# Kernel tuning notes

Hardware: AMD Instinct MI355X
Metric: run time of the kernel (lower is better)

Reference implementation:

```python
import jax, jax.numpy as jnp
import numpy as np

B, C, H, W = 32, 512, 32, 32
CI = C // 2  # inter_channels
EPS = 1e-5


def setup_inputs() -> dict:
    key = jax.random.key(0)
    ks = jax.random.split(key, 12)
    s = 0.02
    return {
        "x": jax.random.normal(ks[0], (B, C, H, W), jnp.float32),
        "w_g": jax.random.normal(ks[1], (CI, C), jnp.float32) * s,
        "b_g": jax.random.normal(ks[2], (CI,), jnp.float32) * s,
        "w_theta": jax.random.normal(ks[3], (CI, C), jnp.float32) * s,
        "b_theta": jax.random.normal(ks[4], (CI,), jnp.float32) * s,
        "w_phi": jax.random.normal(ks[5], (CI, C), jnp.float32) * s,
        "b_phi": jax.random.normal(ks[6], (CI,), jnp.float32) * s,
        "w_W": jax.random.normal(ks[7], (C, CI), jnp.float32) * s,
        "b_W": jax.random.normal(ks[8], (C,), jnp.float32) * s,
        "bn_gamma": jax.random.normal(ks[9], (C,), jnp.float32) * 0.1 + 1.0,
        "bn_beta": jax.random.normal(ks[10], (C,), jnp.float32) * 0.1,
        "bn_mean": jax.random.normal(ks[11], (C,), jnp.float32) * 0.1,
        "bn_var": jnp.abs(jax.random.normal(jax.random.fold_in(key, 99), (C,), jnp.float32)) * 0.5 + 0.5,
    }


def reference(x, w_g, b_g, w_theta, b_theta, w_phi, b_phi, w_W, b_W,
              bn_gamma, bn_beta, bn_mean, bn_var):
    b, c, h, w = x.shape
    n = h * w
    xf = x.reshape(b, c, n)  # [B, C, N]
    # 1x1 convs == per-pixel channel matmuls
    g = jnp.einsum('oc,bcn->bon', w_g, xf) + b_g[:, None]          # [B, Ci, N]
    theta = jnp.einsum('oc,bcn->bon', w_theta, xf) + b_theta[:, None]
    phi = jnp.einsum('oc,bcn->bon', w_phi, xf) + b_phi[:, None]
    # f[b, i, j] = theta_i . phi_j ; scaled by 1/N (softmax-free attention)
    f_div_C = jnp.einsum('bcn,bcm->bnm', theta, phi) / n           # [B, N, N]
    # y[b, c, n] = sum_m f[b, n, m] * g[b, c, m]
    y = jnp.einsum('bnm,bcm->bcn', f_div_C, g)                     # [B, Ci, N]
    # W: 1x1 conv back to C channels + BatchNorm (inference form)
    Wy = jnp.einsum('oi,bin->bon', w_W, y) + b_W[:, None]          # [B, C, N]
    inv_std = jax.lax.rsqrt(bn_var + EPS)
    bn = (Wy - bn_mean[:, None]) * (inv_std * bn_gamma)[:, None] + bn_beta[:, None]
    z = bn.reshape(b, c, h, w) + x
    return z
```

## Files before the change

kernel.cpp:

```cpp
#include <hip/hip_runtime.h>
#include <hip/hip_bf16.h>
#include <cstdint>
#include <cstddef>

using bf16 = __hip_bfloat16;
typedef __attribute__((ext_vector_type(8))) short short8v;
typedef __attribute__((ext_vector_type(4))) float f32x4;

static constexpr int BATCH = 32;
static constexpr int CH    = 512;
static constexpr int CIc   = 256;
static constexpr int NSP   = 1024;
#define EPSV 1e-5f

__device__ __forceinline__ bf16 f2bf(float f) { return __float2bfloat16(f); }

__device__ __forceinline__ void gload_lds16(const bf16* g, bf16* l) {
  __builtin_amdgcn_global_load_lds(
      (const __attribute__((address_space(1))) void*)g,
      (__attribute__((address_space(3))) void*)l, 16, 0, 0);
}

__global__ __launch_bounds__(256) void convert_weights(
    const float* __restrict__ wg, const float* __restrict__ wph, const float* __restrict__ wth,
    const float* __restrict__ bg, const float* __restrict__ bph, const float* __restrict__ bth,
    const float* __restrict__ wW,
    bf16* __restrict__ wcat, bf16* __restrict__ wWb, float* __restrict__ biascat)
{
  int i = blockIdx.x * 256 + threadIdx.x;
  const int WSZ = CIc * CH;
  if (i < WSZ) {
    wcat[i]         = f2bf(wg[i]);
    wcat[WSZ + i]   = f2bf(wph[i]);
    wcat[2*WSZ + i] = f2bf(wth[i]);
    wWb[i]          = f2bf(wW[i]);
  }
  if (i < CIc) {
    biascat[i]        = bg[i];
    biascat[CIc + i]  = bph[i];
    biascat[2*CIc + i]= bth[i];
  }
}

__global__ __launch_bounds__(256) void transpose_x_kernel(
    const float* __restrict__ x, bf16* __restrict__ xt)
{
  __shared__ bf16 t[32][34];
  int n0 = blockIdx.x * 32, c0 = blockIdx.y * 32, b = blockIdx.z;
  const float* s = x + (size_t)b * CH * NSP;
  bf16* d = xt + (size_t)b * NSP * CH;
  int tx = threadIdx.x & 31, ty = threadIdx.x >> 5;
  #pragma unroll
  for (int i = 0; i < 32; i += 8)
    t[ty + i][tx] = f2bf(s[(size_t)(c0 + ty + i) * NSP + n0 + tx]);
  __syncthreads();
  #pragma unroll
  for (int i = 0; i < 32; i += 8)
    d[(size_t)(n0 + ty + i) * CH + c0 + tx] = t[tx][ty + i];
}

template<int EPI>
__global__ __launch_bounds__(256) void gemm_nt(
    const bf16* __restrict__ A, size_t sA,
    const bf16* __restrict__ Bm, size_t sB,
    void* __restrict__ Cm, size_t sC,
    int M, int N, int K,
    const float* __restrict__ bias,
    bf16* __restrict__ Tt, size_t sT,
    const float* __restrict__ bW, const float* __restrict__ gma,
    const float* __restrict__ bta, const float* __restrict__ mu,
    const float* __restrict__ var,
    const float* __restrict__ xres, size_t sX)
{
  __shared__ bf16 As[2][128 * 64];
  __shared__ bf16 Bs[2][128 * 64];
  const int b  = blockIdx.z;
  const int m0 = blockIdx.y * 128;
  const int n0 = blockIdx.x * 128;
  const bf16* Ab = A  + (size_t)b * sA;
  const bf16* Bb = Bm + (size_t)b * sB;
  const int tid  = threadIdx.x;
  const int wv   = tid >> 6, lane = tid & 63;
  const int l16  = lane & 15, g4 = lane >> 4;
  const int wr   = wv >> 1,  wc = wv & 1;

  f32x4 acc[4][4];
  #pragma unroll
  for (int i = 0; i < 4; ++i)
    #pragma unroll
    for (int j = 0; j < 4; ++j)
      acc[i][j] = (f32x4){0.f, 0.f, 0.f, 0.f};

  auto stage = [&](int ks, int p) {
    #pragma unroll
    for (int i = 0; i < 4; ++i) {
      int s = i * 256 + tid;
      int row = s >> 3, ch8 = (s & 7) << 3;
      gload_lds16(Ab + (size_t)(m0 + row) * K + ks + ch8, &As[p][(i * 256 + wv * 64) * 8]);
      gload_lds16(Bb + (size_t)(n0 + row) * K + ks + ch8, &Bs[p][(i * 256 + wv * 64) * 8]);
    }
  };

  const int nt = K >> 6;
  stage(0, 0);
  __syncthreads();
  for (int t = 0; t < nt; ++t) {
    const int cur = t & 1;
    if (t + 1 < nt) stage((t + 1) << 6, cur ^ 1);
    #pragma unroll
    for (int kk = 0; kk < 2; ++kk) {
      short8v af[4], bfv[4];
      #pragma unroll
      for (int mf = 0; mf < 4; ++mf)
        af[mf] = *(const short8v*)&As[cur][(wr * 64 + mf * 16 + l16) * 64 + kk * 32 + g4 * 8];
      #pragma unroll
      for (int nf = 0; nf < 4; ++nf)
        bfv[nf] = *(const short8v*)&Bs[cur][(wc * 64 + nf * 16 + l16) * 64 + kk * 32 + g4 * 8];
      #pragma unroll
      for (int mf = 0; mf < 4; ++mf)
        #pragma unroll
        for (int nf = 0; nf < 4; ++nf)
          acc[mf][nf] = __builtin_amdgcn_mfma_f32_16x16x32_bf16(af[mf], bfv[nf], acc[mf][nf], 0, 0, 0);
    }
    __syncthreads();
  }

  const int colbase = n0 + wc * 64 + l16;
  const int rowbase = m0 + wr * 64 + g4 * 4;

  if constexpr (EPI == 2) {
    #pragma unroll
    for (int mf = 0; mf < 4; ++mf) {
      #pragma unroll
      for (int j = 0; j < 4; ++j) {
        int row = rowbase + mf * 16 + j;
        float a  = gma[row] * rsqrtf(var[row] + EPSV);
        float bb = (bW[row] - mu[row]) * a + bta[row];
        float sc = a * (1.f / (float)NSP);
        #pragma unroll
        for (int nf = 0; nf < 4; ++nf) {
          int col = colbase + nf * 16;
          ((float*)Cm)[(size_t)b * sC + (size_t)row * N + col] =
              acc[mf][nf][j] * sc + bb + xres[(size_t)b * sX + (size_t)row * N + col];
        }
      }
    }
  } else if constexpr (EPI == 1) {
    if (m0 >= 512) {
      #pragma unroll
      for (int mf = 0; mf < 4; ++mf) {
        int rowt0 = (m0 - 512) + wr * 64 + mf * 16 + g4 * 4;
        #pragma unroll
        for (int nf = 0; nf < 4; ++nf) {
          int col = colbase + nf * 16;
          uint64_t pk = 0;
          #pragma unroll
          for (int j = 0; j < 4; ++j) {
            bf16 bv = f2bf(acc[mf][nf][j] + bias[512 + rowt0 + j]);
            pk |= (uint64_t)(*(unsigned short*)&bv) << (16 * j);
          }
          *(uint64_t*)(Tt + (size_t)b * sT + (size_t)col * CIc + rowt0) = pk;
        }
      }
    } else {
      #pragma unroll
      for (int mf = 0; mf < 4; ++mf)
        #pragma unroll
        for (int j = 0; j < 4; ++j) {
          int row = rowbase + mf * 16 + j;
          float badd = bias[row];
          #pragma unroll
          for (int nf = 0; nf < 4; ++nf) {
            int col = colbase + nf * 16;
            ((bf16*)Cm)[(size_t)b * sC + (size_t)row * N + col] = f2bf(acc[mf][nf][j] + badd);
          }
        }
    }
  } else {
    #pragma unroll
    for (int mf = 0; mf < 4; ++mf)
      #pragma unroll
      for (int j = 0; j < 4; ++j) {
        int row = rowbase + mf * 16 + j;
        #pragma unroll
        for (int nf = 0; nf < 4; ++nf) {
          int col = colbase + nf * 16;
          ((bf16*)Cm)[(size_t)b * sC + (size_t)row * N + col] = f2bf(acc[mf][nf][j]);
        }
      }
  }
}

extern "C" void kernel_launch(void* const* d_in, const int* in_sizes, int n_in,
                              void* d_out, int out_size, void* d_ws, size_t ws_size,
                              hipStream_t stream)
{
  const float* x    = (const float*)d_in[0];
  const float* w_g  = (const float*)d_in[1];
  const float* b_g  = (const float*)d_in[2];
  const float* w_th = (const float*)d_in[3];
  const float* b_th = (const float*)d_in[4];
  const float* w_ph = (const float*)d_in[5];
  const float* b_ph = (const float*)d_in[6];
  const float* w_W  = (const float*)d_in[7];
  const float* b_W  = (const float*)d_in[8];
  const float* gma  = (const float*)d_in[9];
  const float* bta  = (const float*)d_in[10];
  const float* mu   = (const float*)d_in[11];
  const float* var  = (const float*)d_in[12];
  float* out = (float*)d_out;

  char* ws = (char*)d_ws;
  bf16* proj = (bf16*)(ws + 0);
  bf16* xt   = (bf16*)(ws + 33554432);
  bf16* thT  = (bf16*)(ws + 67108864);
  bf16* S    = (bf16*)(ws + 83886080);
  bf16* T    = (bf16*)(ws + 88080384);
  bf16* wcat = (bf16*)(ws + 96468992);
  bf16* wWb  = (bf16*)(ws + 97255424);
  float* bcat= (float*)(ws + 97517568);

  convert_weights<<<512, 256, 0, stream>>>(w_g, w_ph, w_th, b_g, b_ph, b_th, w_W, wcat, wWb, bcat);
  transpose_x_kernel<<<dim3(32, 16, 32), 256, 0, stream>>>(x, xt);

  gemm_nt<1><<<dim3(8, 6, 32), 256, 0, stream>>>(
      wcat, 0, xt, (size_t)NSP * CH, proj, (size_t)CH * NSP,
      768, NSP, CH, bcat, thT, (size_t)NSP * CIc,
      nullptr, nullptr, nullptr, nullptr, nullptr, nullptr, 0);

  gemm_nt<0><<<dim3(2, 2, 32), 256, 0, stream>>>(
      proj + 256 * 1024, (size_t)CH * NSP, proj, (size_t)CH * NSP, S, (size_t)CIc * CIc,
      CIc, CIc, NSP, nullptr, nullptr, 0,
      nullptr, nullptr, nullptr, nullptr, nullptr, nullptr, 0);

  gemm_nt<0><<<dim3(2, 4, 32), 256, 0, stream>>>(
      wWb, 0, S, (size_t)CIc * CIc, T, (size_t)CH * CIc,
      CH, CIc, CIc, nullptr, nullptr, 0,
      nullptr, nullptr, nullptr, nullptr, nullptr, nullptr, 0);

  gemm_nt<2><<<dim3(8, 4, 32), 256, 0, stream>>>(
      T, (size_t)CH * CIc, thT, (size_t)NSP * CIc, out, (size_t)CH * NSP,
      CH, NSP, CIc, nullptr, nullptr, 0,
      b_W, gma, bta, mu, var, x, (size_t)CH * NSP);
}
```

Measured before the change: 138.6 us.

## Use 256x256 tiled 8-wave GEMM with swizzled LDS and split-K-half pipelining

Adds a new 512-thread GEMM kernel with 256x256 output tiles, XOR-swizzled LDS layout, half-tile staged prefetch with explicit vmcnt waits, and MFMA priority hints. It is used for the projection GEMM and the final output GEMM. The projection GEMM now treats batch as part of the N dimension, giving one 128x3 grid over the whole batch. The goal is more data reuse per block and less LDS bank conflict, at the cost of one block per CU and fewer total blocks in the final GEMM (256).

Measured after the change: 135.4 us. -2.3%, faster.

```diff
diff --git a/kernel.cpp b/kernel.cpp
--- a/kernel.cpp
+++ b/kernel.cpp
@@ -60,17 +60,164 @@
 }
 
 template<int EPI>
-__global__ __launch_bounds__(256) void gemm_nt(
+__global__ __launch_bounds__(512, 1) void gemm_nt_256(
     const bf16* __restrict__ A, size_t sA,
     const bf16* __restrict__ Bm, size_t sB,
-    void* __restrict__ Cm, size_t sC,
-    int M, int N, int K,
+    void* __restrict__ Cm,
+    int K,
     const float* __restrict__ bias,
-    bf16* __restrict__ Tt, size_t sT,
+    bf16* __restrict__ Tt,
     const float* __restrict__ bW, const float* __restrict__ gma,
     const float* __restrict__ bta, const float* __restrict__ mu,
     const float* __restrict__ var,
-    const float* __restrict__ xres, size_t sX)
+    const float* __restrict__ xres)
+{
+  __shared__ bf16 As[2][2][256][32];
+  __shared__ bf16 Bs[2][2][256][32];
+  const int zb = blockIdx.z;
+  const int m0 = blockIdx.y * 256;
+  const int n0 = blockIdx.x * 256;
+  const bf16* Ab = A  + (size_t)zb * sA;
+  const bf16* Bb = Bm + (size_t)zb * sB;
+  const int tid  = threadIdx.x;
+  const int wv   = tid >> 6, lane = tid & 63;
+  const int l16  = lane & 15, g4 = lane >> 4;
+  const int wr   = wv >> 2,  wc = wv & 3;
+
+  f32x4 acc[8][4];
+  #pragma unroll
+  for (int i = 0; i < 8; ++i)
+    #pragma unroll
+    for (int j = 0; j < 4; ++j)
+      acc[i][j] = (f32x4){0.f, 0.f, 0.f, 0.f};
+
+  const int swz = ((lane & 3) ^ ((lane >> 3) & 3)) << 3;
+  const int rl  = lane >> 2;
+  auto SH = [&](int tt, int h, int p) {
+    int kbase = tt * 64 + h * 32 + swz;
+    #pragma unroll
+    for (int q = 0; q < 2; ++q) {
+      int r = wv * 32 + q * 16;
+      gload_lds16(Ab + (size_t)(m0 + r + rl) * K + kbase, &As[p][h][r][0]);
+      gload_lds16(Bb + (size_t)(n0 + r + rl) * K + kbase, &Bs[p][h][r][0]);
+    }
+  };
+
+  short8v af[8], bfr[4];
+  const int rslot = (g4 ^ ((l16 >> 1) & 3)) * 8;
+  auto LOADFRAGS = [&](int d, int h) {
+    #pragma unroll
+    for (int mf = 0; mf < 8; ++mf)
+      af[mf] = *(const short8v*)&As[d][h][wr * 128 + mf * 16 + l16][rslot];
+    #pragma unroll
+    for (int nf = 0; nf < 4; ++nf)
+      bfr[nf] = *(const short8v*)&Bs[d][h][wc * 64 + nf * 16 + l16][rslot];
+  };
+  auto MFMAS = [&]() {
+    __builtin_amdgcn_s_setprio(1);
+    #pragma unroll
+    for (int mf = 0; mf < 8; ++mf)
+      #pragma unroll
+      for (int nf = 0; nf < 4; ++nf)
+        acc[mf][nf] = __builtin_amdgcn_mfma_f32_16x16x32_bf16(af[mf], bfr[nf], acc[mf][nf], 0, 0, 0);
+    __builtin_amdgcn_s_setprio(0);
+  };
+
+  const int nt = K >> 6;
+  SH(0, 0, 0); SH(0, 1, 0); SH(1, 0, 1);
+  for (int t = 0; t < nt - 1; ++t) {
+    const int d = t & 1;
+    __builtin_amdgcn_sched_barrier(0);
+    asm volatile("s_waitcnt vmcnt(8)" ::: "memory");
+    __builtin_amdgcn_s_barrier();
+    __builtin_amdgcn_sched_barrier(0);
+    LOADFRAGS(d, 0);
+    SH(t + 1, 1, d ^ 1);
+    MFMAS();
+    __builtin_amdgcn_sched_barrier(0);
+    asm volatile("s_waitcnt vmcnt(8)" ::: "memory");
+    __builtin_amdgcn_s_barrier();
+    __builtin_amdgcn_sched_barrier(0);
+    LOADFRAGS(d, 1);
+    if (t + 2 < nt) SH(t + 2, 0, d);
+    MFMAS();
+    __builtin_amdgcn_sched_barrier(0);
+  }
+  {
+    const int d = (nt - 1) & 1;
+    asm volatile("s_waitcnt vmcnt(4)" ::: "memory");
+    __builtin_amdgcn_s_barrier();
+    __builtin_amdgcn_sched_barrier(0);
+    LOADFRAGS(d, 0);
+    MFMAS();
+    asm volatile("s_waitcnt vmcnt(0)" ::: "memory");
+    __builtin_amdgcn_s_barrier();
+    __builtin_amdgcn_sched_barrier(0);
+    LOADFRAGS(d, 1);
+    MFMAS();
+  }
+
+  const int colbase = n0 + wc * 64 + l16;
+  const int rowb    = wr * 128 + g4 * 4;
+
+  if constexpr (EPI == 2) {
+    #pragma unroll
+    for (int mf = 0; mf < 8; ++mf) {
+      #pragma unroll
+      for (int j = 0; j < 4; ++j) {
+        int row = m0 + rowb + mf * 16 + j;
+        float a  = gma[row] * rsqrtf(var[row] + EPSV);
+        float bb = (bW[row] - mu[row]) * a + bta[row];
+        float sc = a * (1.f / (float)NSP);
+        #pragma unroll
+        for (int nf = 0; nf < 4; ++nf) {
+          int col = colbase + nf * 16;
+          size_t idx = (size_t)zb * (CH * NSP) + (size_t)row * NSP + col;
+          ((float*)Cm)[idx] = acc[mf][nf][j] * sc + bb + ((const float*)xres)[idx];
+        }
+      }
+    }
+  } else {
+    if (m0 < 512) {
+      #pragma unroll
+      for (int mf = 0; mf < 8; ++mf)
+        #pragma unroll
+        for (int j = 0; j < 4; ++j) {
+          int row = m0 + rowb + mf * 16 + j;
+          float badd = bias[row];
+          #pragma unroll
+          for (int nf = 0; nf < 4; ++nf) {
+            int col = colbase + nf * 16;
+            int b = col >> 10, n = col & 1023;
+            ((bf16*)Cm)[(size_t)b * (CH * NSP) + (size_t)row * NSP + n] = f2bf(acc[mf][nf][j] + badd);
+          }
+        }
+    } else {
+      #pragma unroll
+      for (int mf = 0; mf < 8; ++mf) {
+        int ci0 = rowb + mf * 16;
+        #pragma unroll
+        for (int nf = 0; nf < 4; ++nf) {
+          int col = colbase + nf * 16;
+          int b = col >> 10, n = col & 1023;
+          uint64_t pk = 0;
+          #pragma unroll
+          for (int j = 0; j < 4; ++j) {
+            bf16 bv = f2bf(acc[mf][nf][j] + bias[512 + ci0 + j]);
+            pk |= (uint64_t)(*(unsigned short*)&bv) << (16 * j);
+          }
+          *(uint64_t*)(Tt + (size_t)b * (NSP * CIc) + (size_t)n * CIc + ci0) = pk;
+        }
+      }
+    }
+  }
+}
+
+__global__ __launch_bounds__(256) void gemm_nt_small(
+    const bf16* __restrict__ A, size_t sA,
+    const bf16* __restrict__ Bm, size_t sB,
+    bf16* __restrict__ Cm, size_t sC,
+    int N, int K)
 {
   __shared__ bf16 As[2][128 * 64];
   __shared__ bf16 Bs[2][128 * 64];
@@ -127,68 +274,17 @@
 
   const int colbase = n0 + wc * 64 + l16;
   const int rowbase = m0 + wr * 64 + g4 * 4;
-
-  if constexpr (EPI == 2) {
-    #pragma unroll
-    for (int mf = 0; mf < 4; ++mf) {
-      #pragma unroll
-      for (int j = 0; j < 4; ++j) {
-        int row = rowbase + mf * 16 + j;
-        float a  = gma[row] * rsqrtf(var[row] + EPSV);
-        float bb = (bW[row] - mu[row]) * a + bta[row];
-        float sc = a * (1.f / (float)NSP);
-        #pragma unroll
-        for (int nf = 0; nf < 4; ++nf) {
-          int col = colbase + nf * 16;
-          ((float*)Cm)[(size_t)b * sC + (size_t)row * N + col] =
-              acc[mf][nf][j] * sc + bb + xres[(size_t)b * sX + (size_t)row * N + col];
-        }
+  #pragma unroll
+  for (int mf = 0; mf < 4; ++mf)
+    #pragma unroll
+    for (int j = 0; j < 4; ++j) {
+      int row = rowbase + mf * 16 + j;
+      #pragma unroll
+      for (int nf = 0; nf < 4; ++nf) {
+        int col = colbase + nf * 16;
+        Cm[(size_t)b * sC + (size_t)row * N + col] = f2bf(acc[mf][nf][j]);
       }
     }
-  } else if constexpr (EPI == 1) {
-    if (m0 >= 512) {
-      #pragma unroll
-      for (int mf = 0; mf < 4; ++mf) {
-        int rowt0 = (m0 - 512) + wr * 64 + mf * 16 + g4 * 4;
-        #pragma unroll
-        for (int nf = 0; nf < 4; ++nf) {
-          int col = colbase + nf * 16;
-          uint64_t pk = 0;
-          #pragma unroll
-          for (int j = 0; j < 4; ++j) {
-            bf16 bv = f2bf(acc[mf][nf][j] + bias[512 + rowt0 + j]);
-            pk |= (uint64_t)(*(unsigned short*)&bv) << (16 * j);
-          }
-          *(uint64_t*)(Tt + (size_t)b * sT + (size_t)col * CIc + rowt0) = pk;
-        }
-      }
-    } else {
-      #pragma unroll
-      for (int mf = 0; mf < 4; ++mf)
-        #pragma unroll
-        for (int j = 0; j < 4; ++j) {
-          int row = rowbase + mf * 16 + j;
-          float badd = bias[row];
-          #pragma unroll
-          for (int nf = 0; nf < 4; ++nf) {
-            int col = colbase + nf * 16;
-            ((bf16*)Cm)[(size_t)b * sC + (size_t)row * N + col] = f2bf(acc[mf][nf][j] + badd);
-          }
-        }
-    }
-  } else {
-    #pragma unroll
-    for (int mf = 0; mf < 4; ++mf)
-      #pragma unroll
-      for (int j = 0; j < 4; ++j) {
-        int row = rowbase + mf * 16 + j;
-        #pragma unroll
-        for (int nf = 0; nf < 4; ++nf) {
-          int col = colbase + nf * 16;
-          ((bf16*)Cm)[(size_t)b * sC + (size_t)row * N + col] = f2bf(acc[mf][nf][j]);
-        }
-      }
-  }
 }
 
 extern "C" void kernel_launch(void* const* d_in, const int* in_sizes, int n_in,
@@ -223,23 +319,19 @@
   convert_weights<<<512, 256, 0, stream>>>(w_g, w_ph, w_th, b_g, b_ph, b_th, w_W, wcat, wWb, bcat);
   transpose_x_kernel<<<dim3(32, 16, 32), 256, 0, stream>>>(x, xt);
 
-  gemm_nt<1><<<dim3(8, 6, 32), 256, 0, stream>>>(
-      wcat, 0, xt, (size_t)NSP * CH, proj, (size_t)CH * NSP,
-      768, NSP, CH, bcat, thT, (size_t)NSP * CIc,
-      nullptr, nullptr, nullptr, nullptr, nullptr, nullptr, 0);
-
-  gemm_nt<0><<<dim3(2, 2, 32), 256, 0, stream>>>(
+  gemm_nt_256<1><<<dim3(128, 3, 1), 512, 0, stream>>>(
+      wcat, 0, xt, 0, proj, CH, bcat, thT,
+      nullptr, nullptr, nullptr, nullptr, nullptr, nullptr);
+
+  gemm_nt_small<<<dim3(2, 2, 32), 256, 0, stream>>>(
       proj + 256 * 1024, (size_t)CH * NSP, proj, (size_t)CH * NSP, S, (size_t)CIc * CIc,
-      CIc, CIc, NSP, nullptr, nullptr, 0,
-      nullptr, nullptr, nullptr, nullptr, nullptr, nullptr, 0);
-
-  gemm_nt<0><<<dim3(2, 4, 32), 256, 0, stream>>>(
+      CIc, NSP);
+
+  gemm_nt_small<<<dim3(2, 4, 32), 256, 0, stream>>>(
       wWb, 0, S, (size_t)CIc * CIc, T, (size_t)CH * CIc,
-      CH, CIc, CIc, nullptr, nullptr, 0,
-      nullptr, nullptr, nullptr, nullptr, nullptr, nullptr, 0);
-
-  gemm_nt<2><<<dim3(8, 4, 32), 256, 0, stream>>>(
-      T, (size_t)CH * CIc, thT, (size_t)NSP * CIc, out, (size_t)CH * NSP,
-      CH, NSP, CIc, nullptr, nullptr, 0,
-      b_W, gma, bta, mu, var, x, (size_t)CH * NSP);
-}
+      CIc, CIc);
+
+  gemm_nt_256<2><<<dim3(4, 2, 32), 512, 0, stream>>>(
+      T, (size_t)CH * CIc, thT, (size_t)NSP * CIc, out, CIc,
+      nullptr, nullptr, b_W, gma, bta, mu, var, x);
+}
```
